# Optimization experiments

Hardware: AMD Instinct MI355X
Metric: run time of the kernel (lower is better)

## Reference

```python
import jax, jax.numpy as jnp
import numpy as np

NUM_COEFF = 32   # num_coeff_per_dim
NUM_POINTS = 64  # Chebyshev collocation points
MAX_ITERS = 10
TOL = 0.01
BATCH, DIM, HID, T_EVAL_N = 512, 256, 512, 16


def T_grid(t, n):
    # Chebyshev T_k(t), k=0..n-1 -> [n, len(t)]
    rows = [jnp.ones_like(t), t]
    for _ in range(2, n):
        rows.append(2.0 * t * rows[-1] - rows[-2])
    return jnp.stack(rows[:n])


def U_grid(t, n):
    rows = [jnp.ones_like(t), 2.0 * t]
    for _ in range(2, n):
        rows.append(2.0 * t * rows[-1] - rows[-2])
    return jnp.stack(rows[:n])


def DT_grid(t, n):
    # d/dt T_k = k * U_{k-1}
    return jnp.vstack([jnp.zeros((1, t.shape[0]), t.dtype),
                       U_grid(t, n - 1) * jnp.arange(1, n, dtype=t.dtype)[:, None]])


def vf_point(t, y, W1, b1, W2, b2):
    # f(t, y) for y [B, D], scalar t
    h = jnp.tanh(y @ W1 + b1 + t)
    return h @ W2 + b2


def vf_grid(t, y, W1, b1, W2, b2):
    # vectorized over Chebyshev points: y [B, D, P], t [P]
    h = jnp.tanh(jnp.einsum('bdp,dh->bhp', y, W1) + b1[None, :, None] + t[None, None, :])
    return jnp.einsum('bhp,hd->bdp', h, W2) + b2[None, :, None]


def setup_inputs() -> dict:
    key = jax.random.key(0)
    ks = jax.random.split(key, 7)
    s1 = 1.0 / np.sqrt(DIM)
    s2 = 1.0 / np.sqrt(HID)
    return {
        'y_init': jax.random.normal(ks[0], (BATCH, DIM), jnp.float32),
        't_eval': jnp.linspace(0.0, 1.0, T_EVAL_N, dtype=jnp.float32),
        'B_init': jax.random.uniform(ks[1], (BATCH, DIM, NUM_COEFF - 2), jnp.float32),
        'W1': jax.random.normal(ks[2], (DIM, HID), jnp.float32) * s1,
        'b1': jax.random.normal(ks[3], (HID,), jnp.float32) * 0.1,
        'W2': jax.random.normal(ks[4], (HID, DIM), jnp.float32) * s2,
        'b2': jax.random.normal(ks[5], (DIM,), jnp.float32) * 0.1,
    }


def _pan_solve(y_init, t_eval, B_init, W1, b1, W2, b2):
    t0, t1 = t_eval[0], t_eval[-1]
    dt = t_eval.dtype
    # time-independent spectral operators
    t_cheb = -jnp.sign(t1 - t0) * jnp.cos(jnp.pi * jnp.arange(NUM_POINTS, dtype=dt) / NUM_POINTS)
    Dt = jnp.diff(jnp.concatenate([t_cheb, jnp.ones((1,), dt)]))
    Phi = T_grid(t_cheb, NUM_COEFF)                        # [N, P]
    DPhi = (2.0 / (t1 - t0)) * DT_grid(t_cheb, NUM_COEFF)  # [N, P]
    inv0 = jnp.linalg.inv(jnp.stack([Phi[0:2, 0], DPhi[0:2, 0]]).T)  # [2,2]
    PD2 = jnp.stack([Phi[2:, 0], DPhi[2:, 0]], axis=-1)    # [N-2, 2]
    D01 = jnp.stack([DPhi[0, :], DPhi[1, :]], axis=0)      # [2, P]
    Phi_b = DPhi[2:, :] - PD2 @ inv0 @ D01                 # [N-2, P]
    Q = jnp.linalg.inv(Phi_b @ (Dt[:, None] * Phi_b.T))    # [N-2, N-2]
    PhibTQ = (Dt[:, None] * Phi_b.T) @ Q                   # [P, N-2]
    M2 = inv0 @ D01 @ PhibTQ                               # [2, N-2]

    f_init = vf_point(t0, y_init, W1, b1, W2, b2)
    yf2 = jnp.stack([y_init, f_init], axis=-1)             # [B, D, 2]

    def head(B_tail):
        return (yf2 - B_tail @ PD2) @ inv0                 # [B, D, 2]

    B = B_init
    done = jnp.array(False)
    delta = jnp.array(jnp.inf, dt)
    iters = jnp.array(0, jnp.int32)
    for _ in range(MAX_ITERS):  # Picard fixed-point iteration (masked early stop)
        B_prev = B
        B_full = jnp.concatenate([head(B_prev), B_prev], axis=-1)  # [B, D, N]
        y_grid = jnp.einsum('bdn,np->bdp', B_full, Phi)            # [B, D, P]
        fapprox = vf_grid(t_cheb, y_grid, W1, b1, W2, b2)          # [B, D, P]
        B_new = jnp.einsum('bdp,pn->bdn', fapprox, PhibTQ) - yf2 @ M2
        d = jnp.linalg.norm(B_new - B_prev)
        B = jnp.where(done, B_prev, B_new)
        delta = jnp.where(done, delta, d)
        iters = jnp.where(done, iters, iters + 1)
        done = done | (d < TOL)

    B_full = jnp.concatenate([head(B), B], axis=-1)
    t_out = -1.0 + 2.0 * (t_eval - t0) / (t1 - t0)
    Phi_out = T_grid(t_out, NUM_COEFF)                     # [N, T]
    traj = jnp.einsum('bdn,nt->tbd', B_full, Phi_out)      # [T, B, D]
    return traj, B, delta, iters


def reference(y_init, t_eval, B_init, W1, b1, W2, b2):
    traj, B, delta, iters = _pan_solve(y_init, t_eval, B_init, W1, b1, W2, b2)
    return (t_eval, traj, delta, B)
```

## Files before the change

kernel.cpp:

```cpp
#include <hip/hip_runtime.h>
#include <math.h>

#define NBATCH 512
#define NDIM 256
#define NHID 512
#define NC 32
#define NTAIL 30
#define NP 64
#define TEV 16
#define MAXIT 10
#define TOLF 0.01f
#define PI_F 3.14159265358979323846f

typedef __bf16 bf16_t;
typedef __bf16 bf16x8 __attribute__((ext_vector_type(8)));
typedef float f32x4 __attribute__((ext_vector_type(4)));
typedef unsigned short ushort_t;

constexpr size_t OFF_TCHEB = 0;
constexpr size_t OFF_PHIT  = 64;
constexpr size_t OFF_PD2I  = 2112;
constexpr size_t OFF_M2    = 2176;
constexpr size_t OFF_INV0  = 2240;
constexpr size_t OFF_PHIOUT= 2256;
constexpr size_t OFF_PQ    = 2768;
constexpr size_t OFF_PQBH  = 4816;
constexpr size_t OFF_PQBL  = 5840;
constexpr size_t OFF_PHIH  = 6864;
constexpr size_t OFF_PHIL  = 7888;
constexpr size_t OFF_SCAL  = 8912;
constexpr size_t OFF_H1F   = 8928;
constexpr size_t OFF_YF2I  = OFF_H1F + 262144;
constexpr size_t OFF_YM2   = OFF_YF2I + 262144;
constexpr size_t OFF_BT    = OFF_YM2 + 3932160;
constexpr size_t OFF_W1T   = OFF_BT + 3932160;
constexpr size_t OFF_W2T   = OFF_W1T + 65536;
constexpr size_t WS_FLOATS = OFF_W2T + 65536;

constexpr size_t OUT_TEVAL = 0;
constexpr size_t OUT_TRAJ  = 16;
constexpr size_t OUT_DELTA = 16 + (size_t)TEV*NBATCH*NDIM;
constexpr size_t OUT_B     = OUT_DELTA + 1;

__device__ __forceinline__ ushort_t bf16bits(float v) {
    bf16_t h = (bf16_t)v; ushort_t u; __builtin_memcpy(&u, &h, 2); return u;
}
__device__ __forceinline__ float bf16val(ushort_t u) {
    bf16_t h; __builtin_memcpy(&h, &u, 2); return (float)h;
}

__global__ void setup_kernel(const float* __restrict__ t_eval, float* __restrict__ ws,
                             float* __restrict__ out)
{
    __shared__ float Phi[32][64];
    __shared__ float DPhi[32][64];
    __shared__ float Phib[30][64];
    __shared__ float tcs[64];
    __shared__ float DtS[64];
    __shared__ float inv0s[4];
    __shared__ float pd2s[30][2];
    __shared__ double Gaug[30][61];
    __shared__ double rowk[60];
    __shared__ double colk[30];

    const int tid = threadIdx.x;
    const float t0 = t_eval[0], t1 = t_eval[TEV-1];
    const float sgn = (t1 > t0) ? 1.f : -1.f;

    if (tid < 64) {
        const float t = -sgn * cosf(PI_F * (float)tid / 64.f);
        tcs[tid] = t;
        float p0 = 1.f, p1 = t;
        Phi[0][tid] = p0; Phi[1][tid] = p1;
        for (int k = 2; k < 32; ++k) { float pk = 2.f*t*p1 - p0; Phi[k][tid] = pk; p0 = p1; p1 = pk; }
        const float sc = 2.f / (t1 - t0);
        float u0 = 1.f, u1 = 2.f*t;
        DPhi[0][tid] = 0.f;
        DPhi[1][tid] = sc * 1.f * u0;
        DPhi[2][tid] = sc * 2.f * u1;
        for (int k = 3; k < 32; ++k) { float uk = 2.f*t*u1 - u0; DPhi[k][tid] = sc * (float)k * uk; u0 = u1; u1 = uk; }
    }
    __syncthreads();
    if (tid < 64) DtS[tid] = ((tid < 63) ? tcs[tid+1] : 1.0f) - tcs[tid];
    if (tid == 0) {
        double a = Phi[0][0], b = DPhi[0][0], c = Phi[1][0], d = DPhi[1][0];
        double det = a*d - b*c;
        inv0s[0] = (float)( d/det); inv0s[1] = (float)(-b/det);
        inv0s[2] = (float)(-c/det); inv0s[3] = (float)( a/det);
    }
    __syncthreads();
    if (tid == 0) { ws[OFF_INV0+0]=inv0s[0]; ws[OFF_INV0+1]=inv0s[1]; ws[OFF_INV0+2]=inv0s[2]; ws[OFF_INV0+3]=inv0s[3]; }
    if (tid < 30) {
        float P = Phi[2+tid][0], D = DPhi[2+tid][0];
        float a0 = P*inv0s[0] + D*inv0s[2];
        float a1 = P*inv0s[1] + D*inv0s[3];
        pd2s[tid][0] = a0; pd2s[tid][1] = a1;
        ws[OFF_PD2I + tid*2+0] = a0;
        ws[OFF_PD2I + tid*2+1] = a1;
    }
    __syncthreads();
    if (tid < 64)
        for (int m = 0; m < 30; ++m)
            Phib[m][tid] = DPhi[2+m][tid] - (pd2s[m][0]*DPhi[0][tid] + pd2s[m][1]*DPhi[1][tid]);
    __syncthreads();

    for (int e = tid; e < 900; e += 256) {
        int i = e / 30, j = e % 30;
        double s = 0.0;
        for (int p = 0; p < 64; ++p) s += (double)Phib[i][p] * (double)DtS[p] * (double)Phib[j][p];
        Gaug[i][j] = s;
        Gaug[i][30+j] = (i == j) ? 1.0 : 0.0;
    }
    __syncthreads();

    for (int k = 0; k < 30; ++k) {
        double invpv = 1.0 / Gaug[k][k];
        if (tid < 60) rowk[tid] = Gaug[k][tid] * invpv;
        if (tid >= 64 && tid < 94) colk[tid-64] = Gaug[tid-64][k];
        __syncthreads();
        for (int e = tid; e < 1800; e += 256) {
            int i = e / 60, j = e - i*60;
            if (i == k) Gaug[i][j] = rowk[j];
            else        Gaug[i][j] -= colk[i] * rowk[j];
        }
        __syncthreads();
    }

    if (tid < 64) {
        ushort_t* pqh = (ushort_t*)(ws + OFF_PQBH);
        ushort_t* pql = (ushort_t*)(ws + OFF_PQBL);
        float pqrow[32];
        for (int n = 0; n < 30; ++n) {
            double s = 0.0;
            for (int m = 0; m < 30; ++m) s += (double)Phib[m][tid] * Gaug[m][30+n];
            pqrow[n] = (float)((double)DtS[tid] * s);
        }
        pqrow[30] = 0.f; pqrow[31] = 0.f;
        for (int n = 0; n < 32; ++n) {
            ws[OFF_PQ + (size_t)tid*32 + n] = pqrow[n];
            bf16_t h = (bf16_t)pqrow[n];
            float hf = (float)h;
            pqh[n*64 + tid] = bf16bits(pqrow[n]);
            pql[n*64 + tid] = bf16bits(pqrow[n] - hf);
        }
    }
    __syncthreads();

    if (tid < 30) {
        double a20 = 0.0, a21 = 0.0;
        for (int p = 0; p < 64; ++p) {
            double pq = (double)ws[OFF_PQ + (size_t)p*32 + tid];
            a20 += (double)DPhi[0][p] * pq;
            a21 += (double)DPhi[1][p] * pq;
        }
        ws[OFF_M2 + 0*32 + tid] = (float)((double)inv0s[0]*a20 + (double)inv0s[1]*a21);
        ws[OFF_M2 + 1*32 + tid] = (float)((double)inv0s[2]*a20 + (double)inv0s[3]*a21);
    }

    if (tid < 64) {
        ushort_t* phh = (ushort_t*)(ws + OFF_PHIH);
        ushort_t* phl = (ushort_t*)(ws + OFF_PHIL);
        for (int n = 0; n < 32; ++n) {
            float f = Phi[n][tid];
            ws[OFF_PHIT + (size_t)tid*32 + n] = f;
            ushort_t hb = bf16bits(f);
            phh[tid*32 + n] = hb;
            phl[tid*32 + n] = bf16bits(f - bf16val(hb));
        }
        ws[OFF_TCHEB + tid] = tcs[tid];
    }

    if (tid < TEV) {
        float te = t_eval[tid];
        out[OUT_TEVAL + tid] = te;
        float tt = -1.f + 2.f*(te - t0)/(t1 - t0);
        float q0 = 1.f, q1 = tt;
        ws[OFF_PHIOUT + (size_t)tid*32 + 0] = q0;
        ws[OFF_PHIOUT + (size_t)tid*32 + 1] = q1;
        for (int k = 2; k < 32; ++k) { float qk = 2.f*tt*q1 - q0; ws[OFF_PHIOUT + (size_t)tid*32 + k] = qk; q0 = q1; q1 = qk; }
    }

    if (tid == 0) {
        double* acc = (double*)(ws + OFF_SCAL);
        acc[0] = 0.0;
        int* ip = (int*)(ws + OFF_SCAL + 2);
        ip[0] = 0;
        ip[1] = 0;
    }
}

__global__ __launch_bounds__(256) void transB_kernel(const float* __restrict__ Bin, float* __restrict__ Bt)
{
    const int t = threadIdx.x, b = blockIdx.x;
    const float* src = Bin + ((size_t)(b*NDIM + t)) * NTAIL;
    #pragma unroll
    for (int n = 0; n < NTAIL; ++n)
        Bt[((size_t)b*NTAIL + n)*NDIM + t] = src[n];
}

__global__ __launch_bounds__(256) void transW_kernel(const float* __restrict__ W, bf16_t* __restrict__ Wt,
                                                     int R, int C)
{
    __shared__ float Ls[64][65];
    const int r0 = blockIdx.x*64, c0 = blockIdx.y*64;
    const int lr = threadIdx.x >> 6, lc = threadIdx.x & 63;
    #pragma unroll
    for (int i = 0; i < 16; ++i) {
        int rr = i*4 + lr;
        Ls[rr][lc] = W[(size_t)(r0+rr)*C + c0+lc];
    }
    __syncthreads();
    #pragma unroll
    for (int i = 0; i < 16; ++i) {
        int cc = i*4 + lr;
        Wt[(size_t)(c0+cc)*R + r0 + lc] = (bf16_t)Ls[lc][cc];
    }
}

__global__ __launch_bounds__(512) void finit_h_kernel(const float* __restrict__ y, const float* __restrict__ W1,
                                                      const float* __restrict__ b1, const float* __restrict__ t_eval,
                                                      float* __restrict__ h1)
{
    __shared__ float ys[NDIM];
    const int t = threadIdx.x, b = blockIdx.x;
    if (t < NDIM) ys[t] = y[(size_t)b*NDIM + t];
    __syncthreads();
    float acc = b1[t] + t_eval[0];
    for (int d = 0; d < NDIM; ++d) acc += ys[d] * W1[(size_t)d*NHID + t];
    h1[(size_t)b*NHID + t] = tanhf(acc);
}

__global__ __launch_bounds__(256) void finit_rest_kernel(const float* __restrict__ y, const float* __restrict__ W2,
                                                         const float* __restrict__ b2, const float* __restrict__ h1,
                                                         const float* __restrict__ inv0, const float* __restrict__ M2,
                                                         float* __restrict__ yf2i, float* __restrict__ yM2)
{
    __shared__ float hs[NHID];
    const int t = threadIdx.x, b = blockIdx.x;
    hs[t] = h1[(size_t)b*NHID + t];
    hs[t+256] = h1[(size_t)b*NHID + 256 + t];
    __syncthreads();
    float f = b2[t];
    for (int h = 0; h < NHID; ++h) f += hs[h] * W2[(size_t)h*NDIM + t];
    const float yv = y[(size_t)b*NDIM + t];
    yf2i[((size_t)b*2 + 0)*NDIM + t] = yv*inv0[0] + f*inv0[2];
    yf2i[((size_t)b*2 + 1)*NDIM + t] = yv*inv0[1] + f*inv0[3];
    #pragma unroll
    for (int n = 0; n < NTAIL; ++n)
        yM2[((size_t)b*NTAIL + n)*NDIM + t] = yv*M2[n] + f*M2[32 + n];
}

__global__ __launch_bounds__(256, 2) void iter_kernel(
    const float* __restrict__ pd2i, const float* __restrict__ yf2i, const float* __restrict__ tch,
    const bf16_t* __restrict__ W1t, const bf16_t* __restrict__ W2t,
    const float* __restrict__ b1f, const float* __restrict__ b2f,
    const ushort_t* __restrict__ PQhi, const ushort_t* __restrict__ PQlo,
    const ushort_t* __restrict__ phiH, const ushort_t* __restrict__ phiL,
    const float* __restrict__ yM2, float* __restrict__ Bt,
    double* __restrict__ accum, int* __restrict__ counter,
    int* __restrict__ done, float* __restrict__ outDelta)
{
    if (*done) return;
    __shared__ float pd2s[32][2];
    __shared__ float tchS[64];
    __shared__ double redd[4];
    __shared__ __align__(16) char smemA[33792];
    __shared__ __align__(16) char smemB[17408];
    __shared__ __align__(16) ushort_t PQHs[32*72];
    __shared__ __align__(16) ushort_t PQLs[32*72];

    const int t = threadIdx.x;
    const int b = blockIdx.x;
    const int lane = t & 63, w = t >> 6;
    const int fr = lane & 15, quad = lane >> 4;

    if (t < 60) ((float*)pd2s)[t] = pd2i[t];
    if (t >= 64 && t < 128) tchS[t-64] = tch[t-64];
    {
        int e = t * 8;
        int r = e >> 6, c = e & 63;
        uint4 vh = *(const uint4*)(PQhi + e);
        uint4 vl = *(const uint4*)(PQlo + e);
        *(uint4*)(PQHs + r*72 + c) = vh;
        *(uint4*)(PQLs + r*72 + c) = vl;
    }
    __syncthreads();

    {
        float cf[32];
        #pragma unroll
        for (int n = 0; n < NTAIL; ++n) cf[2+n] = Bt[((size_t)b*NTAIL + n)*NDIM + t];
        float c0 = yf2i[((size_t)b*2 + 0)*NDIM + t];
        float c1 = yf2i[((size_t)b*2 + 1)*NDIM + t];
        #pragma unroll
        for (int n = 0; n < NTAIL; ++n) { c0 -= cf[2+n]*pd2s[n][0]; c1 -= cf[2+n]*pd2s[n][1]; }
        cf[0] = c0; cf[1] = c1;
        unsigned* BH32 = (unsigned*)smemA;
        unsigned* BL32 = (unsigned*)(smemA + 16384);
        #pragma unroll
        for (int n2 = 0; n2 < 16; ++n2) {
            float f0 = cf[2*n2], f1 = cf[2*n2+1];
            ushort_t h0 = bf16bits(f0), h1 = bf16bits(f1);
            ushort_t l0 = bf16bits(f0 - bf16val(h0)), l1 = bf16bits(f1 - bf16val(h1));
            int idx = t*16 + ((n2 >> 2) ^ (t & 3))*4 + (n2 & 3);
            BH32[idx] = (unsigned)h0 | ((unsigned)h1 << 16);
            BL32[idx] = (unsigned)l0 | ((unsigned)l1 << 16);
        }
    }
    __syncthreads();

    ushort_t* Ay = (ushort_t*)smemA;
    {
        bf16x8 bH[4], bL[4];
        const ushort_t* BHu = (const ushort_t*)smemA;
        const ushort_t* BLu = (const ushort_t*)(smemA + 16384);
        #pragma unroll
        for (int j = 0; j < 4; ++j) {
            const int d = w*64 + j*16 + fr;
            const int off = d*32 + (quad ^ (d & 3))*8;
            bH[j] = *(const bf16x8*)(BHu + off);
            bL[j] = *(const bf16x8*)(BLu + off);
        }
        bf16x8 aH[4], aL[4];
        #pragma unroll
        for (int i = 0; i < 4; ++i) {
            aH[i] = *(const bf16x8*)(phiH + (i*16 + fr)*32 + quad*8);
            aL[i] = *(const bf16x8*)(phiL + (i*16 + fr)*32 + quad*8);
        }
        __syncthreads();
        f32x4 accY[4][4];
        #pragma unroll
        for (int i = 0; i < 4; ++i)
            #pragma unroll
            for (int j = 0; j < 4; ++j) {
                f32x4 a = (f32x4){0.f,0.f,0.f,0.f};
                a = __builtin_amdgcn_mfma_f32_16x16x32_bf16(aH[i], bH[j], a, 0, 0, 0);
                a = __builtin_amdgcn_mfma_f32_16x16x32_bf16(aH[i], bL[j], a, 0, 0, 0);
                a = __builtin_amdgcn_mfma_f32_16x16x32_bf16(aL[i], bH[j], a, 0, 0, 0);
                accY[i][j] = a;
            }
        #pragma unroll
        for (int i = 0; i < 4; ++i)
            #pragma unroll
            for (int j = 0; j < 4; ++j)
                #pragma unroll
                for (int r = 0; r < 4; ++r) {
                    const int p = i*16 + quad*4 + r;
                    const int d = w*64 + j*16 + fr;
                    Ay[p*264 + d] = bf16bits(accY[i][j][r]);
                }
    }
    __syncthreads();

    ushort_t* Hc = (ushort_t*)smemB;
    f32x4 accF[4][4];
    #pragma unroll
    for (int i = 0; i < 4; ++i)
        #pragma unroll
        for (int j = 0; j < 4; ++j) accF[i][j] = (f32x4){0.f,0.f,0.f,0.f};

    #pragma unroll
    for (int pass = 0; pass < 4; ++pass) {
        bf16x8 w2f[4][4];
        #pragma unroll
        for (int kt4 = 0; kt4 < 4; ++kt4)
            #pragma unroll
            for (int j = 0; j < 4; ++j) {
                const int d = w*64 + j*16 + fr;
                w2f[kt4][j] = *(const bf16x8*)(W2t + (size_t)d*NHID + pass*128 + kt4*32 + quad*8);
            }
        f32x4 acc1[4][2];
        #pragma unroll
        for (int i = 0; i < 4; ++i)
            #pragma unroll
            for (int j = 0; j < 2; ++j) acc1[i][j] = (f32x4){0.f,0.f,0.f,0.f};
        #pragma unroll
        for (int kt = 0; kt < NDIM; kt += 32) {
            bf16x8 af[4], bfj[2];
            #pragma unroll
            for (int i = 0; i < 4; ++i)
                af[i] = *(const bf16x8*)(Ay + (i*16 + fr)*264 + kt + quad*8);
            #pragma unroll
            for (int j = 0; j < 2; ++j) {
                const int ncol = pass*128 + w*32 + j*16 + fr;
                bfj[j] = *(const bf16x8*)(W1t + (size_t)ncol*NDIM + kt + quad*8);
            }
            #pragma unroll
            for (int i = 0; i < 4; ++i)
                #pragma unroll
                for (int j = 0; j < 2; ++j)
                    acc1[i][j] = __builtin_amdgcn_mfma_f32_16x16x32_bf16(af[i], bfj[j], acc1[i][j], 0, 0, 0);
        }
        __syncthreads();
        #pragma unroll
        for (int i = 0; i < 4; ++i)
            #pragma unroll
            for (int j = 0; j < 2; ++j) {
                const int col = w*32 + j*16 + fr;
                const float bv = b1f[pass*128 + col];
                #pragma unroll
                for (int r = 0; r < 4; ++r) {
                    const int row = i*16 + quad*4 + r;
                    float v = acc1[i][j][r] + bv + tchS[row];
                    v = fminf(fmaxf(v, -15.f), 15.f);
                    float e = __expf(2.f*v);
                    Hc[row*136 + col] = bf16bits((e - 1.f)/(e + 1.f));
                }
            }
        __syncthreads();
        #pragma unroll
        for (int kt4 = 0; kt4 < 4; ++kt4) {
            bf16x8 af[4];
            #pragma unroll
            for (int i = 0; i < 4; ++i)
                af[i] = *(const bf16x8*)(Hc + (i*16 + fr)*136 + kt4*32 + quad*8);
            #pragma unroll
            for (int i = 0; i < 4; ++i)
                #pragma unroll
                for (int j = 0; j < 4; ++j)
                    accF[i][j] = __builtin_amdgcn_mfma_f32_16x16x32_bf16(af[i], w2f[kt4][j], accF[i][j], 0, 0, 0);
        }
    }
    __syncthreads();

    {
        unsigned* FsT32 = (unsigned*)smemA;
        #pragma unroll
        for (int i = 0; i < 4; ++i)
            #pragma unroll
            for (int j = 0; j < 4; ++j) {
                const int d = w*64 + j*16 + fr;
                const float bv = b2f[d];
                #pragma unroll
                for (int rp = 0; rp < 2; ++rp) {
                    unsigned u0 = bf16bits(accF[i][j][rp*2]   + bv);
                    unsigned u1 = bf16bits(accF[i][j][rp*2+1] + bv);
                    FsT32[d*33 + i*8 + quad*2 + rp] = u0 | (u1 << 16);
                }
            }
    }
    __syncthreads();

    double ss = 0.0;
    {
        const ushort_t* FsTu = (const ushort_t*)smemA;
        f32x4 acc2[2][4];
        #pragma unroll
        for (int m2 = 0; m2 < 2; ++m2)
            #pragma unroll
            for (int j2 = 0; j2 < 4; ++j2) acc2[m2][j2] = (f32x4){0.f,0.f,0.f,0.f};
        #pragma unroll
        for (int kk = 0; kk < 2; ++kk) {
            bf16x8 ah[2], al[2];
            #pragma unroll
            for (int m2 = 0; m2 < 2; ++m2) {
                const int off = (m2*16 + fr)*72 + kk*32 + quad*8;
                ah[m2] = *(const bf16x8*)(PQHs + off);
                al[m2] = *(const bf16x8*)(PQLs + off);
            }
            #pragma unroll
            for (int j2 = 0; j2 < 4; ++j2) {
                const int d2 = w*64 + j2*16 + fr;
                bf16x8 bfv = *(const bf16x8*)(FsTu + d2*66 + kk*32 + quad*8);
                #pragma unroll
                for (int m2 = 0; m2 < 2; ++m2) {
                    acc2[m2][j2] = __builtin_amdgcn_mfma_f32_16x16x32_bf16(ah[m2], bfv, acc2[m2][j2], 0, 0, 0);
                    acc2[m2][j2] = __builtin_amdgcn_mfma_f32_16x16x32_bf16(al[m2], bfv, acc2[m2][j2], 0, 0, 0);
                }
            }
        }
        #pragma unroll
        for (int m2 = 0; m2 < 2; ++m2)
            #pragma unroll
            for (int j2 = 0; j2 < 4; ++j2)
                #pragma unroll
                for (int rr = 0; rr < 4; ++rr) {
                    const int n = m2*16 + quad*4 + rr;
                    if (n < NTAIL) {
                        const int d = w*64 + j2*16 + fr;
                        const size_t idx = ((size_t)b*NTAIL + n)*NDIM + d;
                        float val = acc2[m2][j2][rr] - yM2[idx];
                        float old = Bt[idx];
                        float diff = val - old;
                        Bt[idx] = val;
                        ss += (double)diff*(double)diff;
                    }
                }
    }

    #pragma unroll
    for (int off = 32; off > 0; off >>= 1) ss += __shfl_down(ss, off, 64);
    if (lane == 0) redd[w] = ss;
    __syncthreads();
    if (t == 0) {
        double tot = redd[0] + redd[1] + redd[2] + redd[3];
        atomicAdd(accum, tot);
        __threadfence();
        int old = atomicAdd(counter, 1);
        if (old == 511) {
            unsigned long long raw = atomicExch((unsigned long long*)accum, 0ull);
            double total; __builtin_memcpy(&total, &raw, 8);
            float dl = (float)sqrt(total);
            *outDelta = dl;
            *counter = 0;
            if (dl < TOLF) *done = 1;
        }
    }
}

__global__ __launch_bounds__(256) void kernelEpi(const float* __restrict__ PhiOut, const float* __restrict__ pd2i,
                                                 const float* __restrict__ yf2i, const float* __restrict__ Bt,
                                                 float* __restrict__ outTraj, float* __restrict__ outB)
{
    __shared__ float Po[16][32];
    const int t = threadIdx.x, b = blockIdx.x;
    for (int i = t; i < 512; i += 256) ((float*)Po)[i] = PhiOut[i];
    __syncthreads();
    float cf[32];
    #pragma unroll
    for (int n = 0; n < NTAIL; ++n) cf[2+n] = Bt[((size_t)b*NTAIL + n)*NDIM + t];
    float c0 = yf2i[((size_t)b*2 + 0)*NDIM + t];
    float c1 = yf2i[((size_t)b*2 + 1)*NDIM + t];
    #pragma unroll
    for (int n = 0; n < NTAIL; ++n) { c0 -= cf[2+n]*pd2i[n*2]; c1 -= cf[2+n]*pd2i[n*2+1]; }
    cf[0] = c0; cf[1] = c1;
    for (int tt = 0; tt < TEV; ++tt) {
        float s = 0.f;
        #pragma unroll
        for (int k = 0; k < 32; ++k) s += cf[k]*Po[tt][k];
        outTraj[((size_t)tt*NBATCH + b)*NDIM + t] = s;
    }
    float* ob = outB + ((size_t)(b*NDIM + t))*NTAIL;
    #pragma unroll
    for (int n = 0; n < NTAIL; ++n) ob[n] = cf[2+n];
}

extern "C" void kernel_launch(void* const* d_in, const int* in_sizes, int n_in,
                              void* d_out, int out_size, void* d_ws, size_t ws_size,
                              hipStream_t stream)
{
    const float* y_init = (const float*)d_in[0];
    const float* t_eval = (const float*)d_in[1];
    const float* B_init = (const float*)d_in[2];
    const float* W1     = (const float*)d_in[3];
    const float* b1     = (const float*)d_in[4];
    const float* W2     = (const float*)d_in[5];
    const float* b2     = (const float*)d_in[6];
    float* out = (float*)d_out;
    float* ws  = (float*)d_ws;
    if (ws_size < WS_FLOATS * sizeof(float)) return;

    float* tcheb = ws + OFF_TCHEB;
    float* pd2i  = ws + OFF_PD2I;
    float* M2    = ws + OFF_M2;
    float* inv0  = ws + OFF_INV0;
    float* PhiOut= ws + OFF_PHIOUT;
    double* accum = (double*)(ws + OFF_SCAL);
    int* done    = (int*)(ws + OFF_SCAL + 2);
    int* counter = (int*)(ws + OFF_SCAL + 3);
    float* h1   = ws + OFF_H1F;
    float* yf2i = ws + OFF_YF2I;
    float* yM2  = ws + OFF_YM2;
    float* Bt   = ws + OFF_BT;
    bf16_t* W1t = (bf16_t*)(ws + OFF_W1T);
    bf16_t* W2t = (bf16_t*)(ws + OFF_W2T);
    ushort_t* pqh = (ushort_t*)(ws + OFF_PQBH);
    ushort_t* pql = (ushort_t*)(ws + OFF_PQBL);
    ushort_t* phh = (ushort_t*)(ws + OFF_PHIH);
    ushort_t* phl = (ushort_t*)(ws + OFF_PHIL);

    setup_kernel<<<1, 256, 0, stream>>>(t_eval, ws, out);
    transB_kernel<<<NBATCH, 256, 0, stream>>>(B_init, Bt);
    transW_kernel<<<dim3(NDIM/64, NHID/64), 256, 0, stream>>>(W1, W1t, NDIM, NHID);
    transW_kernel<<<dim3(NHID/64, NDIM/64), 256, 0, stream>>>(W2, W2t, NHID, NDIM);
    finit_h_kernel<<<NBATCH, 512, 0, stream>>>(y_init, W1, b1, t_eval, h1);
    finit_rest_kernel<<<NBATCH, 256, 0, stream>>>(y_init, W2, b2, h1, inv0, M2, yf2i, yM2);

    for (int it = 0; it < MAXIT; ++it) {
        iter_kernel<<<NBATCH, 256, 0, stream>>>(pd2i, yf2i, tcheb, W1t, W2t, b1, b2,
                                                pqh, pql, phh, phl, yM2, Bt,
                                                accum, counter, done, out + OUT_DELTA);
    }
    kernelEpi<<<NBATCH, 256, 0, stream>>>(PhiOut, pd2i, yf2i, Bt, out + OUT_TRAJ, out + OUT_B);
}
```

Measured before the change: 796.7 us.

## Split iter_kernel work across 8 waves per block instead of 4

```diff
diff --git a/kernel.cpp b/kernel.cpp
--- a/kernel.cpp
+++ b/kernel.cpp
@@ -250,7 +250,7 @@
         yM2[((size_t)b*NTAIL + n)*NDIM + t] = yv*M2[n] + f*M2[32 + n];
 }
 
-__global__ __launch_bounds__(256, 2) void iter_kernel(
+__global__ __launch_bounds__(512, 4) void iter_kernel(
     const float* __restrict__ pd2i, const float* __restrict__ yf2i, const float* __restrict__ tch,
     const bf16_t* __restrict__ W1t, const bf16_t* __restrict__ W2t,
     const float* __restrict__ b1f, const float* __restrict__ b2f,
@@ -263,7 +263,7 @@
     if (*done) return;
     __shared__ float pd2s[32][2];
     __shared__ float tchS[64];
-    __shared__ double redd[4];
+    __shared__ double redd[8];
     __shared__ __align__(16) char smemA[33792];
     __shared__ __align__(16) char smemB[17408];
     __shared__ __align__(16) ushort_t PQHs[32*72];
@@ -276,8 +276,8 @@
 
     if (t < 60) ((float*)pd2s)[t] = pd2i[t];
     if (t >= 64 && t < 128) tchS[t-64] = tch[t-64];
-    {
-        int e = t * 8;
+    if (t >= 256) {
+        int e = (t - 256) * 8;
         int r = e >> 6, c = e & 63;
         uint4 vh = *(const uint4*)(PQhi + e);
         uint4 vl = *(const uint4*)(PQlo + e);
@@ -286,7 +286,7 @@
     }
     __syncthreads();
 
-    {
+    if (t < 256) {
         float cf[32];
         #pragma unroll
         for (int n = 0; n < NTAIL; ++n) cf[2+n] = Bt[((size_t)b*NTAIL + n)*NDIM + t];
@@ -311,12 +311,12 @@
 
     ushort_t* Ay = (ushort_t*)smemA;
     {
-        bf16x8 bH[4], bL[4];
+        bf16x8 bH[2], bL[2];
         const ushort_t* BHu = (const ushort_t*)smemA;
         const ushort_t* BLu = (const ushort_t*)(smemA + 16384);
         #pragma unroll
-        for (int j = 0; j < 4; ++j) {
-            const int d = w*64 + j*16 + fr;
+        for (int j = 0; j < 2; ++j) {
+            const int d = w*32 + j*16 + fr;
             const int off = d*32 + (quad ^ (d & 3))*8;
             bH[j] = *(const bf16x8*)(BHu + off);
             bL[j] = *(const bf16x8*)(BLu + off);
@@ -328,11 +328,11 @@
             aL[i] = *(const bf16x8*)(phiL + (i*16 + fr)*32 + quad*8);
         }
         __syncthreads();
-        f32x4 accY[4][4];
+        f32x4 accY[4][2];
         #pragma unroll
         for (int i = 0; i < 4; ++i)
             #pragma unroll
-            for (int j = 0; j < 4; ++j) {
+            for (int j = 0; j < 2; ++j) {
                 f32x4 a = (f32x4){0.f,0.f,0.f,0.f};
                 a = __builtin_amdgcn_mfma_f32_16x16x32_bf16(aH[i], bH[j], a, 0, 0, 0);
                 a = __builtin_amdgcn_mfma_f32_16x16x32_bf16(aH[i], bL[j], a, 0, 0, 0);
@@ -342,71 +342,65 @@
         #pragma unroll
         for (int i = 0; i < 4; ++i)
             #pragma unroll
-            for (int j = 0; j < 4; ++j)
+            for (int j = 0; j < 2; ++j)
                 #pragma unroll
                 for (int r = 0; r < 4; ++r) {
                     const int p = i*16 + quad*4 + r;
-                    const int d = w*64 + j*16 + fr;
+                    const int d = w*32 + j*16 + fr;
                     Ay[p*264 + d] = bf16bits(accY[i][j][r]);
                 }
     }
     __syncthreads();
 
     ushort_t* Hc = (ushort_t*)smemB;
-    f32x4 accF[4][4];
+    f32x4 accF[4][2];
     #pragma unroll
     for (int i = 0; i < 4; ++i)
         #pragma unroll
-        for (int j = 0; j < 4; ++j) accF[i][j] = (f32x4){0.f,0.f,0.f,0.f};
+        for (int j = 0; j < 2; ++j) accF[i][j] = (f32x4){0.f,0.f,0.f,0.f};
 
     #pragma unroll
     for (int pass = 0; pass < 4; ++pass) {
-        bf16x8 w2f[4][4];
+        bf16x8 w2f[4][2];
         #pragma unroll
         for (int kt4 = 0; kt4 < 4; ++kt4)
             #pragma unroll
-            for (int j = 0; j < 4; ++j) {
-                const int d = w*64 + j*16 + fr;
+            for (int j = 0; j < 2; ++j) {
+                const int d = w*32 + j*16 + fr;
                 w2f[kt4][j] = *(const bf16x8*)(W2t + (size_t)d*NHID + pass*128 + kt4*32 + quad*8);
             }
-        f32x4 acc1[4][2];
-        #pragma unroll
-        for (int i = 0; i < 4; ++i)
-            #pragma unroll
-            for (int j = 0; j < 2; ++j) acc1[i][j] = (f32x4){0.f,0.f,0.f,0.f};
+        f32x4 acc1[4];
+        #pragma unroll
+        for (int i = 0; i < 4; ++i) acc1[i] = (f32x4){0.f,0.f,0.f,0.f};
         #pragma unroll
         for (int kt = 0; kt < NDIM; kt += 32) {
-            bf16x8 af[4], bfj[2];
+            bf16x8 af[4], bfv;
             #pragma unroll
             for (int i = 0; i < 4; ++i)
                 af[i] = *(const bf16x8*)(Ay + (i*16 + fr)*264 + kt + quad*8);
-            #pragma unroll
-            for (int j = 0; j < 2; ++j) {
-                const int ncol = pass*128 + w*32 + j*16 + fr;
-                bfj[j] = *(const bf16x8*)(W1t + (size_t)ncol*NDIM + kt + quad*8);
+            {
+                const int ncol = pass*128 + w*16 + fr;
+                bfv = *(const bf16x8*)(W1t + (size_t)ncol*NDIM + kt + quad*8);
             }
             #pragma unroll
             for (int i = 0; i < 4; ++i)
-                #pragma unroll
-                for (int j = 0; j < 2; ++j)
-                    acc1[i][j] = __builtin_amdgcn_mfma_f32_16x16x32_bf16(af[i], bfj[j], acc1[i][j], 0, 0, 0);
+                acc1[i] = __builtin_amdgcn_mfma_f32_16x16x32_bf16(af[i], bfv, acc1[i], 0, 0, 0);
         }
         __syncthreads();
-        #pragma unroll
-        for (int i = 0; i < 4; ++i)
-            #pragma unroll
-            for (int j = 0; j < 2; ++j) {
-                const int col = w*32 + j*16 + fr;
-                const float bv = b1f[pass*128 + col];
+        {
+            const int col = w*16 + fr;
+            const float bv = b1f[pass*128 + col];
+            #pragma unroll
+            for (int i = 0; i < 4; ++i)
                 #pragma unroll
                 for (int r = 0; r < 4; ++r) {
                     const int row = i*16 + quad*4 + r;
-                    float v = acc1[i][j][r] + bv + tchS[row];
+                    float v = acc1[i][r] + bv + tchS[row];
                     v = fminf(fmaxf(v, -15.f), 15.f);
                     float e = __expf(2.f*v);
                     Hc[row*136 + col] = bf16bits((e - 1.f)/(e + 1.f));
                 }
-            }
+        }
         __syncthreads();
         #pragma unroll
         for (int kt4 = 0; kt4 < 4; ++kt4) {
@@ -417,7 +411,7 @@
             #pragma unroll
             for (int i = 0; i < 4; ++i)
                 #pragma unroll
-                for (int j = 0; j < 4; ++j)
+                for (int j = 0; j < 2; ++j)
                     accF[i][j] = __builtin_amdgcn_mfma_f32_16x16x32_bf16(af[i], w2f[kt4][j], accF[i][j], 0, 0, 0);
         }
     }
@@ -428,8 +422,8 @@
         #pragma unroll
         for (int i = 0; i < 4; ++i)
             #pragma unroll
-            for (int j = 0; j < 4; ++j) {
-                const int d = w*64 + j*16 + fr;
+            for (int j = 0; j < 2; ++j) {
+                const int d = w*32 + j*16 + fr;
                 const float bv = b2f[d];
                 #pragma unroll
                 for (int rp = 0; rp < 2; ++rp) {
@@ -444,11 +438,11 @@
     double ss = 0.0;
     {
         const ushort_t* FsTu = (const ushort_t*)smemA;
-        f32x4 acc2[2][4];
+        f32x4 acc2[2][2];
         #pragma unroll
         for (int m2 = 0; m2 < 2; ++m2)
             #pragma unroll
-            for (int j2 = 0; j2 < 4; ++j2) acc2[m2][j2] = (f32x4){0.f,0.f,0.f,0.f};
+            for (int j2 = 0; j2 < 2; ++j2) acc2[m2][j2] = (f32x4){0.f,0.f,0.f,0.f};
         #pragma unroll
         for (int kk = 0; kk < 2; ++kk) {
             bf16x8 ah[2], al[2];
@@ -459,8 +453,8 @@
                 al[m2] = *(const bf16x8*)(PQLs + off);
             }
             #pragma unroll
-            for (int j2 = 0; j2 < 4; ++j2) {
-                const int d2 = w*64 + j2*16 + fr;
+            for (int j2 = 0; j2 < 2; ++j2) {
+                const int d2 = w*32 + j2*16 + fr;
                 bf16x8 bfv = *(const bf16x8*)(FsTu + d2*66 + kk*32 + quad*8);
                 #pragma unroll
                 for (int m2 = 0; m2 < 2; ++m2) {
@@ -472,12 +466,12 @@
         #pragma unroll
         for (int m2 = 0; m2 < 2; ++m2)
             #pragma unroll
-            for (int j2 = 0; j2 < 4; ++j2)
+            for (int j2 = 0; j2 < 2; ++j2)
                 #pragma unroll
                 for (int rr = 0; rr < 4; ++rr) {
                     const int n = m2*16 + quad*4 + rr;
                     if (n < NTAIL) {
-                        const int d = w*64 + j2*16 + fr;
+                        const int d = w*32 + j2*16 + fr;
                         const size_t idx = ((size_t)b*NTAIL + n)*NDIM + d;
                         float val = acc2[m2][j2][rr] - yM2[idx];
                         float old = Bt[idx];
@@ -493,7 +487,8 @@
     if (lane == 0) redd[w] = ss;
     __syncthreads();
     if (t == 0) {
-        double tot = redd[0] + redd[1] + redd[2] + redd[3];
+        double tot = redd[0] + redd[1] + redd[2] + redd[3]
+                   + redd[4] + redd[5] + redd[6] + redd[7];
         atomicAdd(accum, tot);
         __threadfence();
         int old = atomicAdd(counter, 1);
@@ -577,7 +572,7 @@
     finit_rest_kernel<<<NBATCH, 256, 0, stream>>>(y_init, W2, b2, h1, inv0, M2, yf2i, yM2);
 
     for (int it = 0; it < MAXIT; ++it) {
-        iter_kernel<<<NBATCH, 256, 0, stream>>>(pd2i, yf2i, tcheb, W1t, W2t, b1, b2,
+        iter_kernel<<<NBATCH, 512, 0, stream>>>(pd2i, yf2i, tcheb, W1t, W2t, b1, b2,
                                                 pqh, pql, phh, phl, yM2, Bt,
                                                 accum, counter, done, out + OUT_DELTA);
     }
```

Result: faster. 736.1 us (-7.6%).
